# Performance work log

Hardware: AMD Instinct MI355X
Metric: run time of the kernel (lower is better)

The kernel has to match this reference:

```python
import jax, jax.numpy as jnp
import numpy as np

EMBED_DIM = 1024
NUM_HEADS = 16
HEAD_DIM = EMBED_DIM // NUM_HEADS


def setup_inputs() -> dict:
    key = jax.random.key(0)
    k_x, k_wqkv, k_bqkv, k_wp, k_bp = jax.random.split(key, 5)
    B, S, D = 2, 2048, EMBED_DIM
    bound_qkv = 1.0 / np.sqrt(D)
    bound_p = 1.0 / np.sqrt(D)
    return {
        "x": jax.random.normal(k_x, (B, S, D), dtype=jnp.float32),
        # torch nn.Linear stores weight as (out, in); keep that layout
        "w_qkv": jax.random.uniform(k_wqkv, (3 * D, D), jnp.float32, -bound_qkv, bound_qkv),
        "b_qkv": jax.random.uniform(k_bqkv, (3 * D,), jnp.float32, -bound_qkv, bound_qkv),
        "w_proj": jax.random.uniform(k_wp, (D, D), jnp.float32, -bound_p, bound_p),
        "b_proj": jax.random.uniform(k_bp, (D,), jnp.float32, -bound_p, bound_p),
    }


def reference(x, w_qkv, b_qkv, w_proj, b_proj):
    B, S, D = x.shape
    H, hd = NUM_HEADS, HEAD_DIM
    qkv = x @ w_qkv.T + b_qkv                      # [B,S,3D]
    qkv = qkv.reshape(B, S, 3, H, hd)
    qkv = jnp.transpose(qkv, (2, 0, 3, 1, 4))       # [3,B,H,S,hd]
    q, k, v = qkv[0], qkv[1], qkv[2]
    scale = 1.0 / np.sqrt(hd)
    scores = jnp.einsum('bhqd,bhkd->bhqk', q, k) * scale  # [B,H,S,S]
    attn = jax.nn.softmax(scores, axis=-1)
    out = jnp.einsum('bhqk,bhkd->bhqd', attn, v)    # [B,H,S,hd]
    out = jnp.transpose(out, (0, 2, 1, 3)).reshape(B, S, D)
    return out @ w_proj.T + b_proj
```

## Files before the change

### kernel.cpp

```cpp
#include <hip/hip_runtime.h>
#include <hip/hip_bf16.h>
#include <math.h>


typedef __bf16 bf16_t;
typedef __bf16 bf16x8 __attribute__((ext_vector_type(8)));
typedef __bf16 bf16x4v __attribute__((ext_vector_type(4)));
typedef float f32x4 __attribute__((ext_vector_type(4)));

#define B_ 2
#define S_ 2048
#define D_ 1024
#define H_ 16
#define HD_ 64
#define QSCALE 0.18033688011112042f

__device__ __forceinline__ void load_lds16(const void* g, void* s) {
  __builtin_amdgcn_global_load_lds((__attribute__((address_space(1))) unsigned int*)g,
                                   (__attribute__((address_space(3))) unsigned int*)s,
                                   16, 0, 0);
}

__device__ __forceinline__ float red_sum16(float v) {
  v += __shfl_xor(v, 1);
  v += __shfl_xor(v, 2);
  v += __shfl_xor(v, 4);
  v += __shfl_xor(v, 8);
  return v;
}

__global__ void tobf16_all(const float* __restrict__ x, const float* __restrict__ wq,
                           const float* __restrict__ wp, bf16_t* __restrict__ xb,
                           bf16_t* __restrict__ wqb, bf16_t* __restrict__ wpb) {
  int bid = blockIdx.x;
  const float* in;
  bf16_t* out;
  int base;
  if (bid < 4096) { in = x; out = xb; base = bid; }
  else if (bid < 7168) { in = wq; out = wqb; base = bid - 4096; }
  else { in = wp; out = wpb; base = bid - 7168; }
  int i = base * 256 + threadIdx.x;
  float4 v = ((const float4*)in)[i];
  bf16x4v o;
  o[0] = (bf16_t)v.x; o[1] = (bf16_t)v.y; o[2] = (bf16_t)v.z; o[3] = (bf16_t)v.w;
  ((bf16x4v*)out)[i] = o;
}

template <int EPI, int BN>
__global__ __launch_bounds__(256, 2) void gemm_bt(
    const bf16_t* __restrict__ A, const bf16_t* __restrict__ Bm,
    const float* __restrict__ bias,
    bf16_t* __restrict__ qb, bf16_t* __restrict__ kb, bf16_t* __restrict__ vtb,
    float* __restrict__ outf) {
  constexpr int NI = BN / 32;
  __shared__ __align__(16) bf16_t sA[128 * 32];
  __shared__ __align__(16) bf16_t sB[BN * 32];
  const int tid = threadIdx.x;
  const int w = tid >> 6, lane = tid & 63;
  const int wm = w >> 1, wn = w & 1;
  const int quad = lane >> 4, l15 = lane & 15;
  const int m0 = blockIdx.y * 128, n0 = blockIdx.x * BN;

  f32x4 acc[4][NI];
#pragma unroll
  for (int mi = 0; mi < 4; mi++)
#pragma unroll
    for (int ni = 0; ni < NI; ni++) acc[mi][ni] = (f32x4){0.f, 0.f, 0.f, 0.f};

  for (int kt = 0; kt < 1024; kt += 32) {
    __syncthreads();
#pragma unroll
    for (int i = 0; i < 2; i++) {
      int ub = w * 128 + i * 64;
      int u = ub + lane;
      int r = u >> 2, c = (u & 3) ^ ((r >> 1) & 3);
      load_lds16(A + (size_t)(m0 + r) * 1024 + kt + c * 8, sA + ub * 8);
    }
#pragma unroll
    for (int i = 0; i < BN / 64; i++) {
      int ub = w * (BN / 64) * 64 + i * 64;
      int u = ub + lane;
      int r = u >> 2, c = (u & 3) ^ ((r >> 1) & 3);
      load_lds16(Bm + (size_t)(n0 + r) * 1024 + kt + c * 8, sB + ub * 8);
    }
    __syncthreads();
    bf16x8 af[4], bfr[NI];
#pragma unroll
    for (int mi = 0; mi < 4; mi++) {
      int r = wm * 64 + mi * 16 + l15;
      af[mi] = *(const bf16x8*)(sA + (r * 4 + (quad ^ ((r >> 1) & 3))) * 8);
    }
#pragma unroll
    for (int ni = 0; ni < NI; ni++) {
      int r = wn * (BN / 2) + ni * 16 + l15;
      bfr[ni] = *(const bf16x8*)(sB + (r * 4 + (quad ^ ((r >> 1) & 3))) * 8);
    }
#pragma unroll
    for (int mi = 0; mi < 4; mi++)
#pragma unroll
      for (int ni = 0; ni < NI; ni++)
        acc[mi][ni] = __builtin_amdgcn_mfma_f32_16x16x32_bf16(af[mi], bfr[ni], acc[mi][ni], 0, 0, 0);
  }

#pragma unroll
  for (int mi = 0; mi < 4; mi++) {
#pragma unroll
    for (int ni = 0; ni < NI; ni++) {
      int n = n0 + wn * (BN / 2) + ni * 16 + l15;
      float bv = bias[n];
#pragma unroll
      for (int r = 0; r < 4; r++) {
        int m = m0 + wm * 64 + mi * 16 + quad * 4 + r;
        float v = acc[mi][ni][r] + bv;
        if (EPI == 0) {
          int t = n >> 10;
          int rr = n & 1023;
          int hh = rr >> 6, d = rr & 63;
          int bb = m >> 11, s = m & 2047;
          size_t bh = (size_t)(bb * H_ + hh);
          if (t == 0)
            qb[(bh * S_ + s) * HD_ + d] = (bf16_t)(v * QSCALE);
          else if (t == 1)
            kb[(bh * S_ + s) * HD_ + d] = (bf16_t)v;
          else
            vtb[(bh * HD_ + d) * S_ + s] = (bf16_t)v;
        } else {
          outf[(size_t)m * 1024 + n] = v;
        }
      }
    }
  }
}

__global__ __launch_bounds__(256, 4) void attn(
    const bf16_t* __restrict__ qb, const bf16_t* __restrict__ kb,
    const bf16_t* __restrict__ vtb, bf16_t* __restrict__ ob) {
  __shared__ __align__(16) char smem[40960];
  bf16_t* sP = (bf16_t*)(smem + 32768);
  const int tid = threadIdx.x, w = tid >> 6, lane = tid & 63;
  const int quad = lane >> 4, l15 = lane & 15;
  const int gid = blockIdx.x;
  const int g = gid & 7, k_ = gid >> 3;
  const int bh = g * 4 + (k_ >> 5);
  const int qt = k_ & 31;
  const int b = bh >> 4, h = bh & 15;
  const size_t base = (size_t)bh * S_ * HD_;
  const size_t vbase = (size_t)bh * HD_ * S_;
  const int q0 = qt * 64;

  bf16x8 aq[2];
#pragma unroll
  for (int kk = 0; kk < 2; kk++)
    aq[kk] = *(const bf16x8*)(qb + base + (size_t)(q0 + w * 16 + l15) * 64 + kk * 32 + quad * 8);

  auto stage = [&](int kv0, int bb) {
    char* bK = smem + bb * 16384;
    char* bV = bK + 8192;
#pragma unroll
    for (int i = 0; i < 2; i++) {
      int ub = i * 256 + w * 64;
      int u = ub + lane;
      int rk = u >> 3, ck = (u & 7) ^ (rk & 7);
      load_lds16(kb + base + (size_t)(kv0 + rk) * 64 + ck * 8, bK + (size_t)ub * 16);
      int rv = u >> 3, cv = (u & 7) ^ (rv & 7);
      load_lds16(vtb + vbase + (size_t)rv * S_ + kv0 + cv * 8, bV + (size_t)ub * 16);
    }
  };

  f32x4 acc_o[4];
#pragma unroll
  for (int ni = 0; ni < 4; ni++) acc_o[ni] = (f32x4){0.f, 0.f, 0.f, 0.f};
  float l_part[4] = {0.f, 0.f, 0.f, 0.f};

  stage(0, 0);

  for (int j = 0; j < 32; j++) {
    __syncthreads();
    if (j < 31) stage((j + 1) * 64, (j + 1) & 1);
    const bf16_t* bK = (const bf16_t*)(smem + (j & 1) * 16384);
    const bf16_t* bV = bK + 4096;

    f32x4 s_acc[4];
#pragma unroll
    for (int ni = 0; ni < 4; ni++) s_acc[ni] = (f32x4){0.f, 0.f, 0.f, 0.f};
#pragma unroll
    for (int kk = 0; kk < 2; kk++) {
#pragma unroll
      for (int ni = 0; ni < 4; ni++) {
        int r = ni * 16 + l15, c = kk * 4 + quad;
        bf16x8 bk = *(const bf16x8*)(bK + (r * 8 + (c ^ (r & 7))) * 8);
        s_acc[ni] = __builtin_amdgcn_mfma_f32_16x16x32_bf16(aq[kk], bk, s_acc[ni], 0, 0, 0);
      }
    }

#pragma unroll
    for (int r = 0; r < 4; r++) {
      int row = w * 16 + quad * 4 + r;
      float rs = 0.f;
#pragma unroll
      for (int ni = 0; ni < 4; ni++) {
        float p = exp2f(s_acc[ni][r]);
        rs += p;
        int cu = ni * 2 + (l15 >> 3);
        sP[row * 64 + ((cu ^ (row & 7)) << 3) + (l15 & 7)] = (bf16_t)p;
      }
      l_part[r] += rs;
    }

#pragma unroll
    for (int ks = 0; ks < 2; ks++) {
      int rowA = w * 16 + l15;
      bf16x8 ap = *(const bf16x8*)(sP + (rowA * 8 + ((ks * 4 + quad) ^ (rowA & 7))) * 8);
#pragma unroll
      for (int ni = 0; ni < 4; ni++) {
        int r = ni * 16 + l15, c = ks * 4 + quad;
        bf16x8 bv = *(const bf16x8*)(bV + (r * 8 + (c ^ (r & 7))) * 8);
        acc_o[ni] = __builtin_amdgcn_mfma_f32_16x16x32_bf16(ap, bv, acc_o[ni], 0, 0, 0);
      }
    }
  }

  float inv_l[4];
#pragma unroll
  for (int r = 0; r < 4; r++) inv_l[r] = 1.0f / red_sum16(l_part[r]);

#pragma unroll
  for (int ni = 0; ni < 4; ni++)
#pragma unroll
    for (int r = 0; r < 4; r++) {
      int q = q0 + w * 16 + quad * 4 + r;
      int d = ni * 16 + l15;
      float v = acc_o[ni][r] * inv_l[r];
      ob[((size_t)b * S_ + q) * D_ + h * HD_ + d] = (bf16_t)v;
    }
}

extern "C" void kernel_launch(void* const* d_in, const int* in_sizes, int n_in,
                              void* d_out, int out_size, void* d_ws, size_t ws_size,
                              hipStream_t stream) {
  const float* x = (const float*)d_in[0];
  const float* w_qkv = (const float*)d_in[1];
  const float* b_qkv = (const float*)d_in[2];
  const float* w_proj = (const float*)d_in[3];
  const float* b_proj = (const float*)d_in[4];
  float* out = (float*)d_out;

  char* ws = (char*)d_ws;
  size_t off = 0;
  bf16_t* xb = (bf16_t*)(ws + off); off += (size_t)4096 * 1024 * 2;
  bf16_t* wqkvb = (bf16_t*)(ws + off); off += (size_t)3072 * 1024 * 2;
  bf16_t* wpb = (bf16_t*)(ws + off); off += (size_t)1024 * 1024 * 2;
  bf16_t* qb = (bf16_t*)(ws + off); off += (size_t)4096 * 1024 * 2;
  bf16_t* kb = (bf16_t*)(ws + off); off += (size_t)4096 * 1024 * 2;
  bf16_t* vtb = (bf16_t*)(ws + off); off += (size_t)4096 * 1024 * 2;
  bf16_t* ob = xb;

  tobf16_all<<<8192, 256, 0, stream>>>(x, w_qkv, w_proj, xb, wqkvb, wpb);
  gemm_bt<0, 128><<<dim3(24, 32), 256, 0, stream>>>(xb, wqkvb, b_qkv, qb, kb, vtb, nullptr);
  attn<<<1024, 256, 0, stream>>>(qb, kb, vtb, ob);
  gemm_bt<1, 64><<<dim3(16, 32), 256, 0, stream>>>(ob, wpb, b_proj, nullptr, nullptr, nullptr, out);
}
```

Baseline: 211.5 us.

## Use 32x32 MFMA with 128-query attention tiles and double-buffer GEMM staging

The attention kernel now gives each wave 32 query rows and uses 32x32x16 bf16 MFMAs, with a 128-query tile per block, half as many blocks, and a private P scratch region per wave. This reuses each K/V tile across more queries and lowers LDS fragment traffic per FLOP, at the cost of more accumulator registers and lower occupancy (launch bound 2). The GEMM kernel separately gains a double-buffered LDS stage so the next K-slice is loaded while the current one is computed, which doubles its shared memory use.

```diff
diff --git a/kernel.cpp b/kernel.cpp
--- a/kernel.cpp
+++ b/kernel.cpp
@@ -7,6 +7,7 @@
 typedef __bf16 bf16x8 __attribute__((ext_vector_type(8)));
 typedef __bf16 bf16x4v __attribute__((ext_vector_type(4)));
 typedef float f32x4 __attribute__((ext_vector_type(4)));
+typedef float f32x16 __attribute__((ext_vector_type(16)));
 
 #define B_ 2
 #define S_ 2048
@@ -19,14 +20,6 @@
   __builtin_amdgcn_global_load_lds((__attribute__((address_space(1))) unsigned int*)g,
                                    (__attribute__((address_space(3))) unsigned int*)s,
                                    16, 0, 0);
-}
-
-__device__ __forceinline__ float red_sum16(float v) {
-  v += __shfl_xor(v, 1);
-  v += __shfl_xor(v, 2);
-  v += __shfl_xor(v, 4);
-  v += __shfl_xor(v, 8);
-  return v;
 }
 
 __global__ void tobf16_all(const float* __restrict__ x, const float* __restrict__ wq,
@@ -53,47 +46,57 @@
     bf16_t* __restrict__ qb, bf16_t* __restrict__ kb, bf16_t* __restrict__ vtb,
     float* __restrict__ outf) {
   constexpr int NI = BN / 32;
-  __shared__ __align__(16) bf16_t sA[128 * 32];
-  __shared__ __align__(16) bf16_t sB[BN * 32];
+  constexpr int BUF = 8192 + BN * 64;
+  __shared__ __align__(16) char smem[2 * BUF];
   const int tid = threadIdx.x;
   const int w = tid >> 6, lane = tid & 63;
   const int wm = w >> 1, wn = w & 1;
   const int quad = lane >> 4, l15 = lane & 15;
   const int m0 = blockIdx.y * 128, n0 = blockIdx.x * BN;
 
-  f32x4 acc[4][NI];
-#pragma unroll
-  for (int mi = 0; mi < 4; mi++)
-#pragma unroll
-    for (int ni = 0; ni < NI; ni++) acc[mi][ni] = (f32x4){0.f, 0.f, 0.f, 0.f};
-
-  for (int kt = 0; kt < 1024; kt += 32) {
-    __syncthreads();
+  auto stage = [&](int kt, int bb) {
+    char* bA = smem + bb * BUF;
+    char* bB = bA + 8192;
 #pragma unroll
     for (int i = 0; i < 2; i++) {
       int ub = w * 128 + i * 64;
       int u = ub + lane;
       int r = u >> 2, c = (u & 3) ^ ((r >> 1) & 3);
-      load_lds16(A + (size_t)(m0 + r) * 1024 + kt + c * 8, sA + ub * 8);
+      load_lds16(A + (size_t)(m0 + r) * 1024 + kt + c * 8, bA + (size_t)ub * 16);
     }
 #pragma unroll
     for (int i = 0; i < BN / 64; i++) {
       int ub = w * (BN / 64) * 64 + i * 64;
       int u = ub + lane;
       int r = u >> 2, c = (u & 3) ^ ((r >> 1) & 3);
-      load_lds16(Bm + (size_t)(n0 + r) * 1024 + kt + c * 8, sB + ub * 8);
-    }
+      load_lds16(Bm + (size_t)(n0 + r) * 1024 + kt + c * 8, bB + (size_t)ub * 16);
+    }
+  };
+
+  f32x4 acc[4][NI];
+#pragma unroll
+  for (int mi = 0; mi < 4; mi++)
+#pragma unroll
+    for (int ni = 0; ni < NI; ni++) acc[mi][ni] = (f32x4){0.f, 0.f, 0.f, 0.f};
+
+  stage(0, 0);
+
+  for (int it = 0; it < 32; it++) {
     __syncthreads();
+    if (it < 31) stage((it + 1) * 32, (it + 1) & 1);
+    const bf16_t* bA = (const bf16_t*)(smem + (it & 1) * BUF);
+    const bf16_t* bB = (const bf16_t*)(smem + (it & 1) * BUF + 8192);
+
     bf16x8 af[4], bfr[NI];
 #pragma unroll
     for (int mi = 0; mi < 4; mi++) {
       int r = wm * 64 + mi * 16 + l15;
-      af[mi] = *(const bf16x8*)(sA + (r * 4 + (quad ^ ((r >> 1) & 3))) * 8);
+      af[mi] = *(const bf16x8*)(bA + (r * 4 + (quad ^ ((r >> 1) & 3))) * 8);
     }
 #pragma unroll
     for (int ni = 0; ni < NI; ni++) {
       int r = wn * (BN / 2) + ni * 16 + l15;
-      bfr[ni] = *(const bf16x8*)(sB + (r * 4 + (quad ^ ((r >> 1) & 3))) * 8);
+      bfr[ni] = *(const bf16x8*)(bB + (r * 4 + (quad ^ ((r >> 1) & 3))) * 8);
     }
 #pragma unroll
     for (int mi = 0; mi < 4; mi++)
@@ -132,26 +135,26 @@
   }
 }
 
-__global__ __launch_bounds__(256, 4) void attn(
+__global__ __launch_bounds__(256, 2) void attn(
     const bf16_t* __restrict__ qb, const bf16_t* __restrict__ kb,
     const bf16_t* __restrict__ vtb, bf16_t* __restrict__ ob) {
-  __shared__ __align__(16) char smem[40960];
-  bf16_t* sP = (bf16_t*)(smem + 32768);
+  __shared__ __align__(16) char smem[49152];
   const int tid = threadIdx.x, w = tid >> 6, lane = tid & 63;
-  const int quad = lane >> 4, l15 = lane & 15;
+  const int h2 = lane >> 5, l31 = lane & 31;
   const int gid = blockIdx.x;
   const int g = gid & 7, k_ = gid >> 3;
-  const int bh = g * 4 + (k_ >> 5);
-  const int qt = k_ & 31;
+  const int bh = g * 4 + (k_ >> 4);
+  const int qt = k_ & 15;
   const int b = bh >> 4, h = bh & 15;
   const size_t base = (size_t)bh * S_ * HD_;
   const size_t vbase = (size_t)bh * HD_ * S_;
-  const int q0 = qt * 64;
-
-  bf16x8 aq[2];
-#pragma unroll
-  for (int kk = 0; kk < 2; kk++)
-    aq[kk] = *(const bf16x8*)(qb + base + (size_t)(q0 + w * 16 + l15) * 64 + kk * 32 + quad * 8);
+  const int q0 = qt * 128;
+  char* Pw = smem + 32768 + w * 4096;
+
+  bf16x8 aq[4];
+#pragma unroll
+  for (int ks = 0; ks < 4; ks++)
+    aq[ks] = *(const bf16x8*)(qb + base + (size_t)(q0 + w * 32 + l31) * 64 + ks * 16 + h2 * 8);
 
   auto stage = [&](int kv0, int bb) {
     char* bK = smem + bb * 16384;
@@ -167,10 +170,14 @@
     }
   };
 
-  f32x4 acc_o[4];
-#pragma unroll
-  for (int ni = 0; ni < 4; ni++) acc_o[ni] = (f32x4){0.f, 0.f, 0.f, 0.f};
-  float l_part[4] = {0.f, 0.f, 0.f, 0.f};
+  f32x16 acc_o[2];
+#pragma unroll
+  for (int dt = 0; dt < 2; dt++)
+#pragma unroll
+    for (int i = 0; i < 16; i++) acc_o[dt][i] = 0.f;
+  float l_part[16];
+#pragma unroll
+  for (int i = 0; i < 16; i++) l_part[i] = 0.f;
 
   stage(0, 0);
 
@@ -180,57 +187,65 @@
     const bf16_t* bK = (const bf16_t*)(smem + (j & 1) * 16384);
     const bf16_t* bV = bK + 4096;
 
-    f32x4 s_acc[4];
-#pragma unroll
-    for (int ni = 0; ni < 4; ni++) s_acc[ni] = (f32x4){0.f, 0.f, 0.f, 0.f};
-#pragma unroll
-    for (int kk = 0; kk < 2; kk++) {
-#pragma unroll
-      for (int ni = 0; ni < 4; ni++) {
-        int r = ni * 16 + l15, c = kk * 4 + quad;
-        bf16x8 bk = *(const bf16x8*)(bK + (r * 8 + (c ^ (r & 7))) * 8);
-        s_acc[ni] = __builtin_amdgcn_mfma_f32_16x16x32_bf16(aq[kk], bk, s_acc[ni], 0, 0, 0);
+    f32x16 s_acc[2];
+#pragma unroll
+    for (int nt = 0; nt < 2; nt++)
+#pragma unroll
+      for (int i = 0; i < 16; i++) s_acc[nt][i] = 0.f;
+#pragma unroll
+    for (int ks = 0; ks < 4; ks++) {
+#pragma unroll
+      for (int nt = 0; nt < 2; nt++) {
+        int r = nt * 32 + l31;
+        bf16x8 bk = *(const bf16x8*)(bK + (r * 8 + ((ks * 2 + h2) ^ (r & 7))) * 8);
+        s_acc[nt] = __builtin_amdgcn_mfma_f32_32x32x16_bf16(aq[ks], bk, s_acc[nt], 0, 0, 0);
       }
     }
 
 #pragma unroll
-    for (int r = 0; r < 4; r++) {
-      int row = w * 16 + quad * 4 + r;
-      float rs = 0.f;
-#pragma unroll
-      for (int ni = 0; ni < 4; ni++) {
-        float p = exp2f(s_acc[ni][r]);
-        rs += p;
-        int cu = ni * 2 + (l15 >> 3);
-        sP[row * 64 + ((cu ^ (row & 7)) << 3) + (l15 & 7)] = (bf16_t)p;
+    for (int reg = 0; reg < 16; reg++) {
+      int rr = (reg & 3) + 8 * (reg >> 2) + 4 * h2;
+      float p0 = exp2f(s_acc[0][reg]);
+      float p1 = exp2f(s_acc[1][reg]);
+      l_part[reg] += p0 + p1;
+      int u0 = ((l31 >> 3) ^ (rr & 7));
+      int u1 = (((l31 >> 3) + 4) ^ (rr & 7));
+      *(bf16_t*)(Pw + rr * 128 + u0 * 16 + (l31 & 7) * 2) = (bf16_t)p0;
+      *(bf16_t*)(Pw + rr * 128 + u1 * 16 + (l31 & 7) * 2) = (bf16_t)p1;
+    }
+
+#pragma unroll
+    for (int ks = 0; ks < 4; ks++) {
+      bf16x8 ap = *(const bf16x8*)(Pw + l31 * 128 + (((ks * 2 + h2) ^ (l31 & 7)) * 16));
+#pragma unroll
+      for (int dt = 0; dt < 2; dt++) {
+        int r = dt * 32 + l31;
+        bf16x8 bv = *(const bf16x8*)(bV + (r * 8 + ((ks * 2 + h2) ^ (r & 7))) * 8);
+        acc_o[dt] = __builtin_amdgcn_mfma_f32_32x32x16_bf16(ap, bv, acc_o[dt], 0, 0, 0);
       }
-      l_part[r] += rs;
-    }
-
-#pragma unroll
-    for (int ks = 0; ks < 2; ks++) {
-      int rowA = w * 16 + l15;
-      bf16x8 ap = *(const bf16x8*)(sP + (rowA * 8 + ((ks * 4 + quad) ^ (rowA & 7))) * 8);
-#pragma unroll
-      for (int ni = 0; ni < 4; ni++) {
-        int r = ni * 16 + l15, c = ks * 4 + quad;
-        bf16x8 bv = *(const bf16x8*)(bV + (r * 8 + (c ^ (r & 7))) * 8);
-        acc_o[ni] = __builtin_amdgcn_mfma_f32_16x16x32_bf16(ap, bv, acc_o[ni], 0, 0, 0);
-      }
-    }
-  }
-
-  float inv_l[4];
-#pragma unroll
-  for (int r = 0; r < 4; r++) inv_l[r] = 1.0f / red_sum16(l_part[r]);
-
-#pragma unroll
-  for (int ni = 0; ni < 4; ni++)
-#pragma unroll
-    for (int r = 0; r < 4; r++) {
-      int q = q0 + w * 16 + quad * 4 + r;
-      int d = ni * 16 + l15;
-      float v = acc_o[ni][r] * inv_l[r];
+    }
+  }
+
+  float inv_l[16];
+#pragma unroll
+  for (int reg = 0; reg < 16; reg++) {
+    float v = l_part[reg];
+    v += __shfl_xor(v, 1);
+    v += __shfl_xor(v, 2);
+    v += __shfl_xor(v, 4);
+    v += __shfl_xor(v, 8);
+    v += __shfl_xor(v, 16);
+    inv_l[reg] = 1.0f / v;
+  }
+
+#pragma unroll
+  for (int dt = 0; dt < 2; dt++)
+#pragma unroll
+    for (int reg = 0; reg < 16; reg++) {
+      int rr = (reg & 3) + 8 * (reg >> 2) + 4 * h2;
+      int q = q0 + w * 32 + rr;
+      int d = dt * 32 + l31;
+      float v = acc_o[dt][reg] * inv_l[reg];
       ob[((size_t)b * S_ + q) * D_ + h * HD_ + d] = (bf16_t)v;
     }
 }
@@ -257,6 +272,6 @@
 
   tobf16_all<<<8192, 256, 0, stream>>>(x, w_qkv, w_proj, xb, wqkvb, wpb);
   gemm_bt<0, 128><<<dim3(24, 32), 256, 0, stream>>>(xb, wqkvb, b_qkv, qb, kb, vtb, nullptr);
-  attn<<<1024, 256, 0, stream>>>(qb, kb, vtb, ob);
+  attn<<<512, 256, 0, stream>>>(qb, kb, vtb, ob);
   gemm_bt<1, 64><<<dim3(16, 32), 256, 0, stream>>>(ob, wpb, b_proj, nullptr, nullptr, nullptr, out);
 }
```

After: 207.7 us. No clear change (-1.8%).
